# Kernel optimization log

Measured on AMD Instinct MI355X. Metric: run time of the kernel, lower is better.

The kernel has to match this reference:

```python
import jax, jax.numpy as jnp
import numpy as np

B, S, D_IN, D_OUT = 4, 2048, 1024, 1024

def setup_inputs() -> dict:
    key = jax.random.key(0)
    kx, kq, kk, kv = jax.random.split(key, 4)
    x = jax.random.normal(kx, (B, S, D_IN), dtype=jnp.float32)
    # torch nn.Linear weight is [d_out, d_in]; we store the transposed [d_in, d_out]
    # so y = x @ W, scaled like default init to keep magnitudes sane.
    scale = 1.0 / np.sqrt(D_IN)
    Wq = jax.random.normal(kq, (D_IN, D_OUT), dtype=jnp.float32) * scale
    Wk = jax.random.normal(kk, (D_IN, D_OUT), dtype=jnp.float32) * scale
    Wv = jax.random.normal(kv, (D_IN, D_OUT), dtype=jnp.float32) * scale
    return {"x": x, "Wq": Wq, "Wk": Wk, "Wv": Wv}

def reference(x, Wq, Wk, Wv):
    b, n, _ = x.shape
    q = jnp.einsum('bnd,de->bne', x, Wq)   # [B,S,D_OUT]
    k = jnp.einsum('bnd,de->bne', x, Wk)
    v = jnp.einsum('bnd,de->bne', x, Wv)
    scores = jnp.einsum('bqe,bke->bqk', q, k) / jnp.sqrt(jnp.float32(k.shape[-1]))
    causal = jnp.triu(jnp.ones((n, n), dtype=bool), k=1)  # True above diagonal -> masked
    scores = jnp.where(causal[None, :, :], -jnp.inf, scores)
    weights = jax.nn.softmax(scores, axis=-1)
    # dropout p=0.0 (deterministic baseline) -> identity
    context = jnp.einsum('bqk,bke->bqe', weights, v)
    return context
```

## Files before the change

kernel.cpp:

```cpp
#include <hip/hip_runtime.h>
#include <hip/hip_bf16.h>

#define BB 4
#define SS 2048
#define DD 1024

typedef __attribute__((ext_vector_type(8))) short bf16x8;
typedef __attribute__((ext_vector_type(4))) float f32x4;

__device__ __forceinline__ ushort f2bf(float f) {
  unsigned u = __float_as_uint(f);
  unsigned r = (u + 0x7fffu + ((u >> 16) & 1u)) >> 16;
  return (ushort)r;
}

__device__ __forceinline__ void gload_lds16(const void* g, void* l) {
  __builtin_amdgcn_global_load_lds(
      (const __attribute__((address_space(1))) void*)g,
      (__attribute__((address_space(3))) void*)l, 16, 0, 0);
}

__global__ __launch_bounds__(256) void cast_all(const float* __restrict__ x,
                                                const float* __restrict__ W0,
                                                const float* __restrict__ W1,
                                                const float* __restrict__ W2,
                                                ushort* __restrict__ xb,
                                                ushort* __restrict__ Wt) {
  if (blockIdx.x < 2048) {
    const int i = blockIdx.x * 256 + threadIdx.x;
#pragma unroll
    for (int j = 0; j < 4; j++) {
      const int idx = i + j * 524288;
      const float4 a = ((const float4*)x)[idx];
      ushort4 o;
      o.x = f2bf(a.x); o.y = f2bf(a.y); o.z = f2bf(a.z); o.w = f2bf(a.w);
      ((ushort4*)xb)[idx] = o;
    }
  } else {
    const int b = blockIdx.x - 2048;
    const int z = b >> 10, rem = b & 1023;
    const int bx = rem & 31, by = rem >> 5;
    const float* W = z == 0 ? W0 : (z == 1 ? W1 : W2);
    ushort* O = Wt + (size_t)z * DD * DD;
    __shared__ ushort t[32][33];
    const int n0 = bx * 32, k0 = by * 32;
    const int tx = threadIdx.x & 31, ty = threadIdx.x >> 5;
#pragma unroll
    for (int j = 0; j < 4; j++) {
      int k = k0 + ty + j * 8;
      t[ty + j * 8][tx] = f2bf(W[(size_t)k * DD + n0 + tx]);
    }
    __syncthreads();
#pragma unroll
    for (int j = 0; j < 4; j++) {
      int n = ty + j * 8;
      O[(size_t)(n0 + n) * DD + k0 + tx] = t[tx][n];
    }
  }
}

template <int BM, int BN, int GMODE, bool EXPMASK, bool OUT_BF16>
__global__ __launch_bounds__(512) void gemm8(const ushort* __restrict__ A, int lda, size_t strA,
                                             const ushort* __restrict__ Bt, int ldb, size_t strB,
                                             void* __restrict__ C, int ldc, size_t strC, int K,
                                             int NBX, void* __restrict__ C2) {
  constexpr int LA = BM / 64;
  constexpr int LB = BN / 64;
  constexpr int FM = BM / 32;
  constexpr int FN = BN / 64;
  int nb, mb, bz;
  const ushort* Ab;
  const ushort* Bb;
  void* Cc = C;
  int ldcv = ldc;
  if (GMODE == 2) {
    constexpr int T = 136;
    int flat = blockIdx.x + T * blockIdx.z;
    flat = (flat & 7) * ((T * BB) >> 3) + (flat >> 3);
    bz = flat / T;
    int i = flat % T;
    mb = (int)((sqrtf(8.f * i + 1.f) - 1.f) * 0.5f);
    while ((mb + 1) * (mb + 2) / 2 <= i) ++mb;
    while (mb * (mb + 1) / 2 > i) --mb;
    nb = i - mb * (mb + 1) / 2;
    Ab = A + (size_t)bz * strA;
    Bb = Bt + (size_t)bz * strB;
  } else {
    const int nwg = gridDim.x;
    int L = (blockIdx.x & 7) * (nwg >> 3) + (blockIdx.x >> 3);
    bz = 0;
    if (L < 1024) {
      nb = L & 15; mb = L >> 4;
      Ab = A; Bb = Bt;
    } else {
      int L2 = L - 1024;
      nb = L2 & 63; mb = L2 >> 6;
      Ab = Bt + 2 * DD * DD;
      Bb = A;
      Cc = C2; ldcv = BB * SS;
    }
  }

  __shared__ ushort lds[2][(BM + BN) * 64];

  const int tid = threadIdx.x;
  const int lane = tid & 63;
  const int wid = tid >> 6;
  const int wr = wid >> 2, wc = wid & 3;
  const int fr = lane & 15, qq = lane >> 4;
  const int sx = (fr & 7) << 4;

  const int NT = K >> 6;

  auto stage = [&](int kt, int buf) {
    ushort* As = &lds[buf][0];
    ushort* Bs = &lds[buf][BM * 64];
    const ushort* ga = Ab + (size_t)mb * BM * lda + kt * 64;
    const ushort* gb = Bb + (size_t)nb * BN * ldb + kt * 64;
#pragma unroll
    for (int j = 0; j < LA; j++) {
      int D = (j * 512 + tid) * 16;
      int r = D >> 7;
      int cb = (D & 127) ^ ((r & 7) << 4);
      gload_lds16(ga + (size_t)r * lda + (cb >> 1), (char*)As + D);
    }
#pragma unroll
    for (int j = 0; j < LB; j++) {
      int D = (j * 512 + tid) * 16;
      int r = D >> 7;
      int cb = (D & 127) ^ ((r & 7) << 4);
      gload_lds16(gb + (size_t)r * ldb + (cb >> 1), (char*)Bs + D);
    }
  };

  stage(0, 0);
  if (NT > 1) stage(1, 1);

  f32x4 acc[FM][FN] = {};

  for (int kt = 0; kt < NT; ++kt) {
    const int cur = kt & 1;
    if (kt < NT - 1) {
      if constexpr (LA + LB == 4) asm volatile("s_waitcnt vmcnt(4)" ::: "memory");
      else asm volatile("s_waitcnt vmcnt(0)" ::: "memory");
    } else {
      asm volatile("s_waitcnt vmcnt(0)" ::: "memory");
    }
    __builtin_amdgcn_s_barrier();
    __builtin_amdgcn_sched_barrier(0);

    const char* As = (const char*)&lds[cur][0];
    const char* Bs = (const char*)&lds[cur][BM * 64];
    __builtin_amdgcn_s_setprio(1);
#pragma unroll
    for (int ks = 0; ks < 2; ++ks) {
      const int kb = ks * 64 + qq * 16;
      bf16x8 a[FM], b[FN];
#pragma unroll
      for (int i = 0; i < FM; i++) {
        int r = wr * (BM / 2) + i * 16 + fr;
        a[i] = *(const bf16x8*)(As + r * 128 + (kb ^ sx));
      }
#pragma unroll
      for (int j = 0; j < FN; j++) {
        int r = wc * (BN / 4) + j * 16 + fr;
        b[j] = *(const bf16x8*)(Bs + r * 128 + (kb ^ sx));
      }
#pragma unroll
      for (int i = 0; i < FM; i++)
#pragma unroll
        for (int j = 0; j < FN; j++)
          acc[i][j] = __builtin_amdgcn_mfma_f32_16x16x32_bf16(a[i], b[j], acc[i][j], 0, 0, 0);
    }
    __builtin_amdgcn_s_setprio(0);
    __builtin_amdgcn_s_barrier();
    __builtin_amdgcn_sched_barrier(0);
    if (kt + 2 < NT) stage(kt + 2, cur);
  }

  const int col0 = nb * BN + wc * (BN / 4) + fr;
  const int row00 = mb * BM + wr * (BM / 2) + qq * 4;
  if (OUT_BF16) {
    ushort* Cb = (ushort*)Cc + (size_t)bz * strC;
#pragma unroll
    for (int i = 0; i < FM; i++)
#pragma unroll
      for (int rr = 0; rr < 4; rr++) {
        const int row = row00 + i * 16 + rr;
        size_t ro = (size_t)row * ldcv;
#pragma unroll
        for (int j = 0; j < FN; j++) {
          float v = acc[i][j][rr];
          if (EXPMASK) {
            v = __expf(v * 0.03125f);
            if (col0 + j * 16 > row) v = 0.f;
          }
          Cb[ro + col0 + j * 16] = f2bf(v);
        }
      }
  } else {
    float* Cb = (float*)Cc + (size_t)bz * strC;
#pragma unroll
    for (int i = 0; i < FM; i++)
#pragma unroll
      for (int rr = 0; rr < 4; rr++) {
        size_t ro = (size_t)(row00 + i * 16 + rr) * ldcv;
#pragma unroll
        for (int j = 0; j < FN; j++) Cb[ro + col0 + j * 16] = acc[i][j][rr];
      }
  }
}

__global__ __launch_bounds__(256) void pv_dual(const ushort* __restrict__ P,
                                               const ushort* __restrict__ Vt,
                                               float* __restrict__ out) {
  const int f = blockIdx.x;
  const int xcd = f & 7, L = f >> 3;
  const int bz = xcd >> 1, chalf = xcd & 1;
  const int nd = L & 15, c = chalf * 4 + ((L >> 4) & 3);

  __shared__ ushort lds[2][(128 + 128) * 64];
  __shared__ float lds_l[2][64];

  const int tid = threadIdx.x;
  const int lane = tid & 63, wid = tid >> 6;
  const int wr = wid >> 1, wc = wid & 1;
  const int fr = lane & 15, qq = lane >> 4;
  const int sx = (fr & 7) << 4;

  bf16x8 ones;
#pragma unroll
  for (int e = 0; e < 8; e++) ones[e] = (short)0x3F80;

  const ushort* Pb = P + (size_t)bz * SS * SS;
  const ushort* Bg = Vt + (size_t)bz * 2048 + (size_t)(nd * 64) * 8192;

  auto stageA = [&](int mb, int kt, int buf) {
    ushort* As = &lds[buf][0];
    const ushort* ga = Pb + (size_t)(mb * 128) * SS + kt * 64;
#pragma unroll
    for (int j = 0; j < 4; j++) {
      int D = (j * 256 + tid) * 16;
      int r = D >> 7;
      int cb = (D & 127) ^ ((r & 7) << 4);
      gload_lds16(ga + (size_t)r * SS + (cb >> 1), (char*)As + D);
    }
  };
  auto stageB = [&](int kt, int buf) {
    ushort* Bs = &lds[buf][128 * 64];
    const ushort* gb = Bg + kt * 64;
#pragma unroll
    for (int j = 0; j < 2; j++) {
      int D = (j * 256 + tid) * 16;
      int r = D >> 7;
      int cb = (D & 127) ^ ((r & 7) << 4);
      gload_lds16(gb + (size_t)r * 8192 + (cb >> 1), (char*)Bs + D);
    }
  };

#pragma unroll 1
  for (int ph = 0; ph < 2; ++ph) {
    const int mb = ph == 0 ? c : 15 - c;
    const int NT = 2 * (mb + 1);

    stageA(mb, 0, 0); stageB(0, 0);
    if (NT > 1) { stageA(mb, 1, 1); stageB(1, 1); }

    f32x4 acc[4][2] = {};
    f32x4 accl[4] = {};

    for (int kt = 0; kt < NT; ++kt) {
      const int cur = kt & 1;
      if (kt < NT - 1) asm volatile("s_waitcnt vmcnt(6)" ::: "memory");
      else             asm volatile("s_waitcnt vmcnt(0)" ::: "memory");
      __builtin_amdgcn_s_barrier();
      __builtin_amdgcn_sched_barrier(0);

      const char* As = (const char*)&lds[cur][0];
      const char* Bs = (const char*)&lds[cur][128 * 64];
      __builtin_amdgcn_s_setprio(1);
#pragma unroll
      for (int ks = 0; ks < 2; ++ks) {
        const int kb = ks * 64 + qq * 16;
        bf16x8 a[4], b[2];
#pragma unroll
        for (int i = 0; i < 4; i++) {
          int r = wr * 64 + i * 16 + fr;
          a[i] = *(const bf16x8*)(As + r * 128 + (kb ^ sx));
        }
#pragma unroll
        for (int n = 0; n < 2; n++) {
          int r = wc * 32 + n * 16 + fr;
          b[n] = *(const bf16x8*)(Bs + r * 128 + (kb ^ sx));
        }
        if (wc == 0) {
#pragma unroll
          for (int i = 0; i < 4; i++)
            accl[i] = __builtin_amdgcn_mfma_f32_16x16x32_bf16(a[i], ones, accl[i], 0, 0, 0);
        }
#pragma unroll
        for (int i = 0; i < 4; i++)
#pragma unroll
          for (int n = 0; n < 2; n++)
            acc[i][n] = __builtin_amdgcn_mfma_f32_16x16x32_bf16(a[i], b[n], acc[i][n], 0, 0, 0);
      }
      __builtin_amdgcn_s_setprio(0);
      __builtin_amdgcn_s_barrier();
      __builtin_amdgcn_sched_barrier(0);
      if (kt + 2 < NT) { stageA(mb, kt + 2, cur); stageB(kt + 2, cur); }
    }

    if (wc == 0 && fr == 0) {
#pragma unroll
      for (int i = 0; i < 4; i++)
#pragma unroll
        for (int rr = 0; rr < 4; rr++) lds_l[wr][i * 16 + qq * 4 + rr] = accl[i][rr];
    }
    __syncthreads();

    const int row00 = mb * 128 + wr * 64 + qq * 4;
    float* ob = out + ((size_t)bz * SS) * DD;
#pragma unroll
    for (int i = 0; i < 4; i++)
#pragma unroll
      for (int rr = 0; rr < 4; rr++) {
        const float invl = 1.f / lds_l[wr][i * 16 + qq * 4 + rr];
        float* orow = ob + (size_t)(row00 + i * 16 + rr) * DD + nd * 64 + wc * 32 + fr;
#pragma unroll
        for (int n = 0; n < 2; n++) orow[n * 16] = acc[i][n][rr] * invl;
      }
    __syncthreads();
  }
}

extern "C" void kernel_launch(void* const* d_in, const int* in_sizes, int n_in,
                              void* d_out, int out_size, void* d_ws, size_t ws_size,
                              hipStream_t stream) {
  const float* x = (const float*)d_in[0];
  const float* Wq = (const float*)d_in[1];
  const float* Wk = (const float*)d_in[2];
  const float* Wv = (const float*)d_in[3];

  char* ws = (char*)d_ws;
  ushort* xb = (ushort*)(ws);
  ushort* Wt = (ushort*)(ws + 16777216);
  ushort* QK = (ushort*)(ws + 23068672);
  ushort* Vt = (ushort*)(ws + 56623104);
  ushort* P = (ushort*)(ws + 73400320);

  const size_t S2 = (size_t)SS * SS;
  const size_t SQ2 = (size_t)SS * 2048;

  cast_all<<<5120, 256, 0, stream>>>(x, Wq, Wk, Wv, xb, Wt);
  gemm8<128, 128, 4, false, true><<<dim3(1536), 512, 0, stream>>>(
      xb, DD, 0, Wt, DD, 0, QK, 2048, 0, DD, 16, Vt);
  gemm8<128, 128, 2, true, true><<<dim3(136, 1, BB), 512, 0, stream>>>(
      QK, 2048, SQ2, QK + 1024, 2048, SQ2, P, SS, S2, DD, 0, nullptr);
  pv_dual<<<dim3(512), 256, 0, stream>>>(P, Vt, (float*)d_out);

  (void)in_sizes; (void)n_in; (void)out_size; (void)ws_size;
}
```

Before: 145.6 us.

## Use 256x256 tiled QK projection GEMM and merge V projection into scores kernel

The Q/K projection now runs in a dedicated 256x256-tile GEMM with split-K-half LDS staging and interleaved prefetch/MFMA phases, giving more reuse per loaded byte. The V-transpose projection moves out of that launch and into the scores kernel, which now handles both the causal QK^T tiles and the V^T tiles in one 1056-block grid. The goal is to cut global traffic for the projections and to fill the partially idle causal scores launch with independent work. In exchange, the larger tile uses more registers and LDS per block, and the grid for the projection is only 256 blocks.

```diff
diff --git a/kernel.cpp b/kernel.cpp
--- a/kernel.cpp
+++ b/kernel.cpp
@@ -18,6 +18,11 @@
   __builtin_amdgcn_global_load_lds(
       (const __attribute__((address_space(1))) void*)g,
       (__attribute__((address_space(3))) void*)l, 16, 0, 0);
+}
+
+__device__ __forceinline__ void BARSB() {
+  __builtin_amdgcn_s_barrier();
+  __builtin_amdgcn_sched_barrier(0);
 }
 
 __global__ __launch_bounds__(256) void cast_all(const float* __restrict__ x,
@@ -59,49 +64,157 @@
   }
 }
 
-template <int BM, int BN, int GMODE, bool EXPMASK, bool OUT_BF16>
-__global__ __launch_bounds__(512) void gemm8(const ushort* __restrict__ A, int lda, size_t strA,
-                                             const ushort* __restrict__ Bt, int ldb, size_t strB,
-                                             void* __restrict__ C, int ldc, size_t strC, int K,
-                                             int NBX, void* __restrict__ C2) {
-  constexpr int LA = BM / 64;
-  constexpr int LB = BN / 64;
-  constexpr int FM = BM / 32;
-  constexpr int FN = BN / 64;
-  int nb, mb, bz;
+__global__ __launch_bounds__(512, 2) void gemm256(const ushort* __restrict__ A, int lda,
+                                                  const ushort* __restrict__ Bt, int ldb,
+                                                  ushort* __restrict__ C, int ldc, int K,
+                                                  int NBCOLS) {
+  const int nwg = gridDim.x * gridDim.y;
+  int ord = blockIdx.y * gridDim.x + blockIdx.x;
+  int flat = (ord & 7) * (nwg >> 3) + (ord >> 3);
+  const int mb = flat / NBCOLS, nb = flat % NBCOLS;
+
+  __shared__ char ldsA[2][2][16384];
+  __shared__ char ldsB[2][2][16384];
+
+  const int tid = threadIdx.x;
+  const int lane = tid & 63, wid = tid >> 6;
+  const int wr = wid >> 2, wc = wid & 3;
+  const int fr = lane & 15, qq = lane >> 4;
+  const int kxor = ((qq ^ ((fr >> 1) & 3)) << 4);
+
+  const int srcE = (((tid & 3) ^ ((tid >> 3) & 3)) << 3);
+  const ushort* Ag_t = A + (size_t)(mb * 256 + (tid >> 2)) * lda + srcE;
+  const ushort* Bg_t = Bt + (size_t)(nb * 256 + (tid >> 2)) * ldb + srcE;
+
+  const int NT = K >> 6;
+
+  auto stA = [&](int buf, int kh, int kt) {
+#pragma unroll
+    for (int j = 0; j < 2; j++)
+      gload_lds16(Ag_t + (size_t)(j * 128) * lda + kt * 64 + kh * 32,
+                  &ldsA[buf][kh][(j * 512 + tid) * 16]);
+  };
+  auto stB = [&](int buf, int kh, int kt) {
+#pragma unroll
+    for (int j = 0; j < 2; j++)
+      gload_lds16(Bg_t + (size_t)(j * 128) * ldb + kt * 64 + kh * 32,
+                  &ldsB[buf][kh][(j * 512 + tid) * 16]);
+  };
+  auto ldA8 = [&](int buf, int kh, bf16x8* o) {
+#pragma unroll
+    for (int i = 0; i < 8; i++)
+      o[i] = *(const bf16x8*)(&ldsA[buf][kh][0] + ((wr * 128 + i * 16 + fr) << 6) + kxor);
+  };
+  auto ldB2 = [&](int buf, int kh, int n0, bf16x8* o) {
+#pragma unroll
+    for (int n = 0; n < 2; n++)
+      o[n] = *(const bf16x8*)(&ldsB[buf][kh][0] + ((wc * 64 + (n0 + n) * 16 + fr) << 6) + kxor);
+  };
+
+  f32x4 acc[8][4] = {};
+  bf16x8 a[8], b0[2], b1[2];
+
+#define MF16(BV, NB)                                                           \
+  do {                                                                         \
+    __builtin_amdgcn_s_setprio(1);                                             \
+    _Pragma("unroll") for (int i_ = 0; i_ < 8; i_++) {                         \
+      _Pragma("unroll") for (int n_ = 0; n_ < 2; n_++) {                       \
+        acc[i_][(NB) + n_] = __builtin_amdgcn_mfma_f32_16x16x32_bf16(          \
+            a[i_], BV[n_], acc[i_][(NB) + n_], 0, 0, 0);                       \
+      }                                                                        \
+    }                                                                          \
+    __builtin_amdgcn_s_setprio(0);                                             \
+  } while (0)
+
+  stA(0, 0, 0); stB(0, 0, 0); stA(0, 1, 0); stB(0, 1, 0);
+  __builtin_amdgcn_sched_barrier(0);
+  asm volatile("s_waitcnt vmcnt(4)" ::: "memory");
+  BARSB();
+
+  for (int kt = 0; kt < NT; ++kt) {
+    const int cur = kt & 1, nxt = cur ^ 1;
+    const bool pf = (kt + 1 < NT);
+    ldA8(cur, 0, a);
+    ldB2(cur, 0, 0, b0);
+    if (pf) stA(nxt, 0, kt + 1);
+    MF16(b0, 0);
+    BARSB();
+    ldB2(cur, 0, 2, b1);
+    if (pf) stB(nxt, 0, kt + 1);
+    MF16(b1, 2);
+    __builtin_amdgcn_sched_barrier(0);
+    if (pf) asm volatile("s_waitcnt vmcnt(4)" ::: "memory");
+    else    asm volatile("s_waitcnt vmcnt(0)" ::: "memory");
+    BARSB();
+    ldA8(cur, 1, a);
+    ldB2(cur, 1, 0, b0);
+    if (pf) stA(nxt, 1, kt + 1);
+    MF16(b0, 0);
+    BARSB();
+    ldB2(cur, 1, 2, b1);
+    if (pf) stB(nxt, 1, kt + 1);
+    MF16(b1, 2);
+    __builtin_amdgcn_sched_barrier(0);
+    if (pf) {
+      asm volatile("s_waitcnt vmcnt(4)" ::: "memory");
+      BARSB();
+    }
+  }
+#undef MF16
+
+  const int col0 = nb * 256 + wc * 64 + fr;
+  const int row00 = mb * 256 + wr * 128 + qq * 4;
+#pragma unroll
+  for (int i = 0; i < 8; i++)
+#pragma unroll
+    for (int rr = 0; rr < 4; rr++) {
+      size_t ro = (size_t)(row00 + i * 16 + rr) * ldc;
+#pragma unroll
+      for (int n = 0; n < 4; n++) C[ro + col0 + n * 16] = f2bf(acc[i][n][rr]);
+    }
+}
+
+__global__ __launch_bounds__(512) void scores_vt(const ushort* __restrict__ QK,
+                                                 const ushort* __restrict__ xb,
+                                                 const ushort* __restrict__ Wt,
+                                                 ushort* __restrict__ P,
+                                                 ushort* __restrict__ Vt) {
+  int nb, mb;
   const ushort* Ab;
   const ushort* Bb;
-  void* Cc = C;
-  int ldcv = ldc;
-  if (GMODE == 2) {
+  ushort* Cc;
+  int lda, ldb, ldcv;
+  bool expmask;
+  const int f = blockIdx.x;
+  if (f < 544) {
     constexpr int T = 136;
-    int flat = blockIdx.x + T * blockIdx.z;
-    flat = (flat & 7) * ((T * BB) >> 3) + (flat >> 3);
-    bz = flat / T;
+    int flat = (f & 7) * 68 + (f >> 3);
+    int bz = flat / T;
     int i = flat % T;
     mb = (int)((sqrtf(8.f * i + 1.f) - 1.f) * 0.5f);
     while ((mb + 1) * (mb + 2) / 2 <= i) ++mb;
     while (mb * (mb + 1) / 2 > i) --mb;
     nb = i - mb * (mb + 1) / 2;
-    Ab = A + (size_t)bz * strA;
-    Bb = Bt + (size_t)bz * strB;
+    Ab = QK + (size_t)bz * SS * 2048;
+    Bb = QK + 1024 + (size_t)bz * SS * 2048;
+    lda = ldb = 2048;
+    Cc = P + (size_t)bz * SS * SS;
+    ldcv = SS;
+    expmask = true;
   } else {
-    const int nwg = gridDim.x;
-    int L = (blockIdx.x & 7) * (nwg >> 3) + (blockIdx.x >> 3);
-    bz = 0;
-    if (L < 1024) {
-      nb = L & 15; mb = L >> 4;
-      Ab = A; Bb = Bt;
-    } else {
-      int L2 = L - 1024;
-      nb = L2 & 63; mb = L2 >> 6;
-      Ab = Bt + 2 * DD * DD;
-      Bb = A;
-      Cc = C2; ldcv = BB * SS;
-    }
+    int L = f - 544;
+    int LL = (L & 7) * 64 + (L >> 3);
+    nb = LL & 63;
+    mb = LL >> 6;
+    Ab = Wt + 2 * DD * DD;
+    Bb = xb;
+    lda = ldb = DD;
+    Cc = Vt;
+    ldcv = BB * SS;
+    expmask = false;
   }
 
-  __shared__ ushort lds[2][(BM + BN) * 64];
+  __shared__ ushort lds[2][256 * 64];
 
   const int tid = threadIdx.x;
   const int lane = tid & 63;
@@ -110,22 +223,22 @@
   const int fr = lane & 15, qq = lane >> 4;
   const int sx = (fr & 7) << 4;
 
-  const int NT = K >> 6;
+  const int NT = 16;
 
   auto stage = [&](int kt, int buf) {
     ushort* As = &lds[buf][0];
-    ushort* Bs = &lds[buf][BM * 64];
-    const ushort* ga = Ab + (size_t)mb * BM * lda + kt * 64;
-    const ushort* gb = Bb + (size_t)nb * BN * ldb + kt * 64;
-#pragma unroll
-    for (int j = 0; j < LA; j++) {
+    ushort* Bs = &lds[buf][128 * 64];
+    const ushort* ga = Ab + (size_t)mb * 128 * lda + kt * 64;
+    const ushort* gb = Bb + (size_t)nb * 128 * ldb + kt * 64;
+#pragma unroll
+    for (int j = 0; j < 2; j++) {
       int D = (j * 512 + tid) * 16;
       int r = D >> 7;
       int cb = (D & 127) ^ ((r & 7) << 4);
       gload_lds16(ga + (size_t)r * lda + (cb >> 1), (char*)As + D);
     }
 #pragma unroll
-    for (int j = 0; j < LB; j++) {
+    for (int j = 0; j < 2; j++) {
       int D = (j * 512 + tid) * 16;
       int r = D >> 7;
       int cb = (D & 127) ^ ((r & 7) << 4);
@@ -134,42 +247,38 @@
   };
 
   stage(0, 0);
-  if (NT > 1) stage(1, 1);
-
-  f32x4 acc[FM][FN] = {};
+  stage(1, 1);
+
+  f32x4 acc[4][2] = {};
 
   for (int kt = 0; kt < NT; ++kt) {
     const int cur = kt & 1;
-    if (kt < NT - 1) {
-      if constexpr (LA + LB == 4) asm volatile("s_waitcnt vmcnt(4)" ::: "memory");
-      else asm volatile("s_waitcnt vmcnt(0)" ::: "memory");
-    } else {
-      asm volatile("s_waitcnt vmcnt(0)" ::: "memory");
-    }
+    if (kt < NT - 1) asm volatile("s_waitcnt vmcnt(4)" ::: "memory");
+    else             asm volatile("s_waitcnt vmcnt(0)" ::: "memory");
     __builtin_amdgcn_s_barrier();
     __builtin_amdgcn_sched_barrier(0);
 
     const char* As = (const char*)&lds[cur][0];
-    const char* Bs = (const char*)&lds[cur][BM * 64];
+    const char* Bs = (const char*)&lds[cur][128 * 64];
     __builtin_amdgcn_s_setprio(1);
 #pragma unroll
     for (int ks = 0; ks < 2; ++ks) {
       const int kb = ks * 64 + qq * 16;
-      bf16x8 a[FM], b[FN];
-#pragma unroll
-      for (int i = 0; i < FM; i++) {
-        int r = wr * (BM / 2) + i * 16 + fr;
+      bf16x8 a[4], b[2];
+#pragma unroll
+      for (int i = 0; i < 4; i++) {
+        int r = wr * 64 + i * 16 + fr;
         a[i] = *(const bf16x8*)(As + r * 128 + (kb ^ sx));
       }
 #pragma unroll
-      for (int j = 0; j < FN; j++) {
-        int r = wc * (BN / 4) + j * 16 + fr;
+      for (int j = 0; j < 2; j++) {
+        int r = wc * 32 + j * 16 + fr;
         b[j] = *(const bf16x8*)(Bs + r * 128 + (kb ^ sx));
       }
 #pragma unroll
-      for (int i = 0; i < FM; i++)
-#pragma unroll
-        for (int j = 0; j < FN; j++)
+      for (int i = 0; i < 4; i++)
+#pragma unroll
+        for (int j = 0; j < 2; j++)
           acc[i][j] = __builtin_amdgcn_mfma_f32_16x16x32_bf16(a[i], b[j], acc[i][j], 0, 0, 0);
     }
     __builtin_amdgcn_s_setprio(0);
@@ -178,37 +287,24 @@
     if (kt + 2 < NT) stage(kt + 2, cur);
   }
 
-  const int col0 = nb * BN + wc * (BN / 4) + fr;
-  const int row00 = mb * BM + wr * (BM / 2) + qq * 4;
-  if (OUT_BF16) {
-    ushort* Cb = (ushort*)Cc + (size_t)bz * strC;
-#pragma unroll
-    for (int i = 0; i < FM; i++)
-#pragma unroll
-      for (int rr = 0; rr < 4; rr++) {
-        const int row = row00 + i * 16 + rr;
-        size_t ro = (size_t)row * ldcv;
-#pragma unroll
-        for (int j = 0; j < FN; j++) {
-          float v = acc[i][j][rr];
-          if (EXPMASK) {
-            v = __expf(v * 0.03125f);
-            if (col0 + j * 16 > row) v = 0.f;
-          }
-          Cb[ro + col0 + j * 16] = f2bf(v);
+  const int col0 = nb * 128 + wc * 32 + fr;
+  const int row00 = mb * 128 + wr * 64 + qq * 4;
+#pragma unroll
+  for (int i = 0; i < 4; i++)
+#pragma unroll
+    for (int rr = 0; rr < 4; rr++) {
+      const int row = row00 + i * 16 + rr;
+      size_t ro = (size_t)row * ldcv;
+#pragma unroll
+      for (int j = 0; j < 2; j++) {
+        float v = acc[i][j][rr];
+        if (expmask) {
+          v = __expf(v * 0.03125f);
+          if (col0 + j * 16 > row) v = 0.f;
         }
+        Cc[ro + col0 + j * 16] = f2bf(v);
       }
-  } else {
-    float* Cb = (float*)Cc + (size_t)bz * strC;
-#pragma unroll
-    for (int i = 0; i < FM; i++)
-#pragma unroll
-      for (int rr = 0; rr < 4; rr++) {
-        size_t ro = (size_t)(row00 + i * 16 + rr) * ldcv;
-#pragma unroll
-        for (int j = 0; j < FN; j++) Cb[ro + col0 + j * 16] = acc[i][j][rr];
-      }
-  }
+    }
 }
 
 __global__ __launch_bounds__(256) void pv_dual(const ushort* __restrict__ P,
@@ -348,14 +444,9 @@
   ushort* Vt = (ushort*)(ws + 56623104);
   ushort* P = (ushort*)(ws + 73400320);
 
-  const size_t S2 = (size_t)SS * SS;
-  const size_t SQ2 = (size_t)SS * 2048;
-
   cast_all<<<5120, 256, 0, stream>>>(x, Wq, Wk, Wv, xb, Wt);
-  gemm8<128, 128, 4, false, true><<<dim3(1536), 512, 0, stream>>>(
-      xb, DD, 0, Wt, DD, 0, QK, 2048, 0, DD, 16, Vt);
-  gemm8<128, 128, 2, true, true><<<dim3(136, 1, BB), 512, 0, stream>>>(
-      QK, 2048, SQ2, QK + 1024, 2048, SQ2, P, SS, S2, DD, 0, nullptr);
+  gemm256<<<dim3(8, 32), 512, 0, stream>>>(xb, DD, Wt, DD, QK, 2048, DD, 8);
+  scores_vt<<<dim3(1056), 512, 0, stream>>>(QK, xb, Wt, P, Vt);
   pv_dual<<<dim3(512), 256, 0, stream>>>(P, Vt, (float*)d_out);
 
   (void)in_sizes; (void)n_in; (void)out_size; (void)ws_size;
```

Result: no change. 145.0 us (-0.4%).
